# Performance work log

Hardware: AMD Instinct MI355X
Metric: run time of the kernel (lower is better)

Reference implementation:

```python
import jax, jax.numpy as jnp
import numpy as np

N, F, C1, H, C2, E = 50000, 256, 32, 8, 16, 800000
NEG_SLOPE = 0.2


def gat_layer(x, src, dst, W, a_src, a_dst, b, heads, out_c, concat):
    n = x.shape[0]
    h = (x @ W).reshape(n, heads, out_c)               # [N,H,C]
    al_src = jnp.sum(h * a_src, axis=-1)               # [N,H]
    al_dst = jnp.sum(h * a_dst, axis=-1)               # [N,H]
    e = jax.nn.leaky_relu(al_src[src] + al_dst[dst], NEG_SLOPE)  # [E,H]
    # segment softmax over incoming edges of each dst node
    m = jax.ops.segment_max(e, dst, num_segments=n)
    e = jnp.exp(e - m[dst])
    denom = jax.ops.segment_sum(e, dst, num_segments=n)
    alpha = e / (denom[dst] + 1e-16)                   # [E,H]
    msg = h[src] * alpha[..., None]                    # [E,H,C]
    out = jax.ops.segment_sum(msg, dst, num_segments=n)
    out = out.reshape(n, heads * out_c) if concat else out.mean(axis=1)
    return out + b


def conv1d(x, w, b):
    # x: [1,C,N], w: [O,I,K], 'same' padding (K=5 -> pad 2)
    pad = (w.shape[-1] - 1) // 2
    y = jax.lax.conv_general_dilated(x, w, (1,), [(pad, pad)],
                                     dimension_numbers=('NCH', 'OIH', 'NCH'))
    return y + b[None, :, None]


def setup_inputs() -> dict:
    key = jax.random.key(0)
    ks = jax.random.split(key, 20)
    s = lambda k, shp, sc: jax.random.normal(k, shp, jnp.float32) * sc
    inp = {
        'x': jax.random.normal(ks[0], (N, F), jnp.float32),
        'edge_index': jax.random.randint(ks[1], (2, E), 0, N, jnp.int32),
        'W1': s(ks[2], (F, H * C1), 0.06),
        'a_src1': s(ks[3], (H, C1), 0.1), 'a_dst1': s(ks[4], (H, C1), 0.1),
        'b1': jnp.zeros((H * C1,), jnp.float32),
        'W2': s(ks[5], (H * C1, C2), 0.06),
        'a_src2': s(ks[6], (1, C2), 0.1), 'a_dst2': s(ks[7], (1, C2), 0.1),
        'b2': jnp.zeros((C2,), jnp.float32),
        'proj_w': s(ks[8], (C2, 1), 0.2), 'proj_b': jnp.zeros((1,), jnp.float32),
        'c1_w': s(ks[9], (C2, C2, 5), 0.1), 'c1_b': jnp.zeros((C2,), jnp.float32),
        'c2_w': s(ks[10], (C2, C2, 5), 0.1), 'c2_b': jnp.zeros((C2,), jnp.float32),
        'lin_w': s(ks[11], (2 * C2, C2), 0.15), 'lin_b': jnp.zeros((C2,), jnp.float32),
    }
    return inp


def reference(x, edge_index, W1, a_src1, a_dst1, b1, W2, a_src2, a_dst2, b2,
              proj_w, proj_b, c1_w, c1_b, c2_w, c2_b, lin_w, lin_b):
    n = x.shape[0]
    loops = jnp.arange(n, dtype=edge_index.dtype)
    src = jnp.concatenate([edge_index[0], loops])  # PyG GATConv adds self-loops
    dst = jnp.concatenate([edge_index[1], loops])

    h = jax.nn.relu(gat_layer(x, src, dst, W1, a_src1, a_dst1, b1, H, C1, True))
    x1 = gat_layer(h, src, dst, W2, a_src2, a_dst2, b2, 1, C2, False)  # [N,C2]

    g = (x1 @ proj_w + proj_b)[:, 0]                  # [N]
    sort_idx = jnp.argsort(g)
    inverse_idx = jnp.argsort(sort_idx)
    sorted_x = g[sort_idx][:, None] * x1[sort_idx]    # [N,C2]
    sx = sorted_x.T[None]                             # [1,C2,N]
    sx = jax.nn.relu(conv1d(sx, c1_w, c1_b))
    sx = conv1d(sx, c2_w, c2_b)
    x2 = sx[0].T[inverse_idx]                         # [N,C2]

    out = jnp.concatenate([x1, x2], axis=1) @ lin_w + lin_b
    return jax.nn.log_softmax(out, axis=1)
```

## Files before the change

kernel.cpp:

```cpp
#include <hip/hip_runtime.h>
#include <math.h>

#define NBUCKET 65536

__device__ __forceinline__ float leakyrelu02(float v) { return v > 0.f ? v : 0.2f * v; }

__global__ __launch_bounds__(256) void k_gemm1(const float* __restrict__ A,
                                               const float* __restrict__ B,
                                               float* __restrict__ C, int M) {
  __shared__ float As[16][68];
  const int m0 = blockIdx.x * 64;
  const int n0 = blockIdx.y * 64;
  const int tid = threadIdx.x;
  const int l = tid & 63;
  const int wu = __builtin_amdgcn_readfirstlane(tid >> 6);
  const float* __restrict__ Bw = B + n0 + wu * 16;

  float acc[16];
#pragma unroll
  for (int j = 0; j < 16; ++j) acc[j] = 0.f;

  const int arow = tid & 63, akk = (tid >> 6) * 4;

  for (int k0 = 0; k0 < 256; k0 += 16) {
    float4 av = make_float4(0.f, 0.f, 0.f, 0.f);
    if (m0 + arow < M) av = *(const float4*)(A + (size_t)(m0 + arow) * 256 + k0 + akk);
    As[akk + 0][arow] = av.x;
    As[akk + 1][arow] = av.y;
    As[akk + 2][arow] = av.z;
    As[akk + 3][arow] = av.w;
    __syncthreads();
#pragma unroll
    for (int kk = 0; kk < 16; ++kk) {
      const float* bp = Bw + (size_t)(k0 + kk) * 256;
      float4 b0 = *(const float4*)(bp);
      float4 b1 = *(const float4*)(bp + 4);
      float4 b2 = *(const float4*)(bp + 8);
      float4 b3 = *(const float4*)(bp + 12);
      float a = As[kk][l];
      acc[0] += a * b0.x;  acc[1] += a * b0.y;  acc[2] += a * b0.z;  acc[3] += a * b0.w;
      acc[4] += a * b1.x;  acc[5] += a * b1.y;  acc[6] += a * b1.z;  acc[7] += a * b1.w;
      acc[8] += a * b2.x;  acc[9] += a * b2.y;  acc[10] += a * b2.z; acc[11] += a * b2.w;
      acc[12] += a * b3.x; acc[13] += a * b3.y; acc[14] += a * b3.z; acc[15] += a * b3.w;
    }
    __syncthreads();
  }
  const int m = m0 + l;
  if (m < M) {
    float* cp = C + (size_t)m * 256 + n0 + wu * 16;
    *(float4*)(cp + 0) = make_float4(acc[0], acc[1], acc[2], acc[3]);
    *(float4*)(cp + 4) = make_float4(acc[4], acc[5], acc[6], acc[7]);
    *(float4*)(cp + 8) = make_float4(acc[8], acc[9], acc[10], acc[11]);
    *(float4*)(cp + 12) = make_float4(acc[12], acc[13], acc[14], acc[15]);
  }
}

__global__ __launch_bounds__(256) void k_al1(const float* __restrict__ h_lin,
                                             const float* __restrict__ a_src,
                                             const float* __restrict__ a_dst,
                                             float* __restrict__ als,
                                             float* __restrict__ ald, int N) {
  int gid = blockIdx.x * 256 + threadIdx.x;
  int n = gid >> 6;
  int l = threadIdx.x & 63;
  if (n >= N) return;
  float4 h4 = *(const float4*)(h_lin + (size_t)n * 256 + l * 4);
  float4 vs = *(const float4*)(a_src + l * 4);
  float4 vd = *(const float4*)(a_dst + l * 4);
  float ps = h4.x * vs.x + h4.y * vs.y + h4.z * vs.z + h4.w * vs.w;
  float pd = h4.x * vd.x + h4.y * vd.y + h4.z * vd.z + h4.w * vd.w;
  ps += __shfl_xor(ps, 1); pd += __shfl_xor(pd, 1);
  ps += __shfl_xor(ps, 2); pd += __shfl_xor(pd, 2);
  ps += __shfl_xor(ps, 4); pd += __shfl_xor(pd, 4);
  if ((l & 7) == 0) {
    als[(size_t)n * 8 + (l >> 3)] = ps;
    ald[(size_t)n * 8 + (l >> 3)] = pd;
  }
}

__global__ __launch_bounds__(256) void k_hist(const int* __restrict__ ei,
                                              int* __restrict__ counts, int E, int N) {
  int e = blockIdx.x * 256 + threadIdx.x;
  if (e >= E + N) return;
  int d = (e < E) ? ei[E + e] : (e - E);
  atomicAdd(&counts[d], 1);
}

__global__ __launch_bounds__(1024) void k_scan(const int* __restrict__ counts,
                                               int* __restrict__ offsets,
                                               int* __restrict__ cursor, int chunk) {
  __shared__ int part[1024];
  const int t = threadIdx.x;
  const int base = t * chunk;
  int ssum = 0;
  for (int i = 0; i < chunk; i += 4) {
    int4 v = *(const int4*)(counts + base + i);
    ssum += v.x + v.y + v.z + v.w;
  }
  part[t] = ssum;
  __syncthreads();
  for (int d = 1; d < 1024; d <<= 1) {
    int v = (t >= d) ? part[t - d] : 0;
    __syncthreads();
    part[t] += v;
    __syncthreads();
  }
  int run = (t == 0) ? 0 : part[t - 1];
  for (int i = 0; i < chunk; i += 4) {
    int4 v = *(const int4*)(counts + base + i);
    int4 o;
    o.x = run; run += v.x;
    o.y = run; run += v.y;
    o.z = run; run += v.z;
    o.w = run; run += v.w;
    *(int4*)(offsets + base + i) = o;
    if (cursor) *(int4*)(cursor + base + i) = o;
  }
  if (t == 1023) offsets[1024 * chunk] = run;
}

__global__ __launch_bounds__(256) void k_scatter_ew(
    const int* __restrict__ ei, const float* __restrict__ als1,
    const float* __restrict__ ald1, int* __restrict__ cursor,
    int* __restrict__ csr_src, int* __restrict__ csr_dst,
    float* __restrict__ ew, int E, int N) {
  int e = blockIdx.x * 256 + threadIdx.x;
  if (e >= E + N) return;
  int d, s;
  if (e < E) { d = ei[E + e]; s = ei[e]; }
  else { d = e - E; s = d; }
  int pos = atomicAdd(&cursor[d], 1);
  csr_src[pos] = s;
  csr_dst[pos] = d;
  float4 as0 = *(const float4*)(als1 + (size_t)s * 8);
  float4 as1 = *(const float4*)(als1 + (size_t)s * 8 + 4);
  float4 ad0 = *(const float4*)(ald1 + (size_t)d * 8);
  float4 ad1 = *(const float4*)(ald1 + (size_t)d * 8 + 4);
  float4 w0, w1;
  w0.x = expf(leakyrelu02(as0.x + ad0.x));
  w0.y = expf(leakyrelu02(as0.y + ad0.y));
  w0.z = expf(leakyrelu02(as0.z + ad0.z));
  w0.w = expf(leakyrelu02(as0.w + ad0.w));
  w1.x = expf(leakyrelu02(as1.x + ad1.x));
  w1.y = expf(leakyrelu02(as1.y + ad1.y));
  w1.z = expf(leakyrelu02(as1.z + ad1.z));
  w1.w = expf(leakyrelu02(as1.w + ad1.w));
  *(float4*)(ew + (size_t)pos * 8) = w0;
  *(float4*)(ew + (size_t)pos * 8 + 4) = w1;
}

__global__ __launch_bounds__(256) void k_ew2(const int* __restrict__ csr_src,
                                             const int* __restrict__ csr_dst,
                                             const float* __restrict__ als2,
                                             const float* __restrict__ ald2,
                                             float* __restrict__ ew2, int Etot) {
  int t = blockIdx.x * 256 + threadIdx.x;
  if (t >= Etot) return;
  ew2[t] = expf(leakyrelu02(als2[csr_src[t]] + ald2[csr_dst[t]]));
}

#define RB(i) ((i) + ((i) >> 3))

__global__ __launch_bounds__(256) void k_gat1(
    const float* __restrict__ h_lin, const float* __restrict__ ew,
    const float* __restrict__ b1, const int* __restrict__ offsets,
    const int* __restrict__ csr_src, const float* __restrict__ W2,
    const float* __restrict__ a_src2, const float* __restrict__ a_dst2,
    float* __restrict__ h2, float* __restrict__ als2, float* __restrict__ ald2, int N) {
  __shared__ float rowbuf[4][292];

  const int w = threadIdx.x >> 6;
  const int l = threadIdx.x & 63;
  const int half = l >> 5;
  const int li = l & 31;
  const int h3 = li >> 2;
  const int n = blockIdx.x * 4 + w;
  if (n >= N) return;

  const int off = offsets[n];
  const int deg = offsets[n + 1] - off;
  const float* hb = h_lin + li * 8;

  float c0 = 0.f, c1 = 0.f, c2 = 0.f, c3 = 0.f, c4 = 0.f, c5 = 0.f, c6 = 0.f, c7 = 0.f;
  float sw = 0.f;
  int e = 0;
  for (; e + 8 <= deg; e += 8) {
    const int p0 = off + e + half;
    int s0 = csr_src[p0];
    int s1 = csr_src[p0 + 2];
    int s2 = csr_src[p0 + 4];
    int s3 = csr_src[p0 + 6];
    float w0 = ew[(size_t)p0 * 8 + h3];
    float w1 = ew[(size_t)(p0 + 2) * 8 + h3];
    float w2v = ew[(size_t)(p0 + 4) * 8 + h3];
    float w3 = ew[(size_t)(p0 + 6) * 8 + h3];
    const float* r0p = hb + (size_t)s0 * 256;
    const float* r1p = hb + (size_t)s1 * 256;
    const float* r2p = hb + (size_t)s2 * 256;
    const float* r3p = hb + (size_t)s3 * 256;
    float4 r0a = *(const float4*)(r0p), r0b = *(const float4*)(r0p + 4);
    float4 r1a = *(const float4*)(r1p), r1b = *(const float4*)(r1p + 4);
    float4 r2a = *(const float4*)(r2p), r2b = *(const float4*)(r2p + 4);
    float4 r3a = *(const float4*)(r3p), r3b = *(const float4*)(r3p + 4);
    sw += (w0 + w1) + (w2v + w3);
    c0 += w0 * r0a.x + w1 * r1a.x + w2v * r2a.x + w3 * r3a.x;
    c1 += w0 * r0a.y + w1 * r1a.y + w2v * r2a.y + w3 * r3a.y;
    c2 += w0 * r0a.z + w1 * r1a.z + w2v * r2a.z + w3 * r3a.z;
    c3 += w0 * r0a.w + w1 * r1a.w + w2v * r2a.w + w3 * r3a.w;
    c4 += w0 * r0b.x + w1 * r1b.x + w2v * r2b.x + w3 * r3b.x;
    c5 += w0 * r0b.y + w1 * r1b.y + w2v * r2b.y + w3 * r3b.y;
    c6 += w0 * r0b.z + w1 * r1b.z + w2v * r2b.z + w3 * r3b.z;
    c7 += w0 * r0b.w + w1 * r1b.w + w2v * r2b.w + w3 * r3b.w;
  }
  for (; e < deg; e += 2) {
    int ee = e + half;
    if (ee < deg) {
      int p = off + ee;
      int s = csr_src[p];
      float ww = ew[(size_t)p * 8 + h3];
      const float* rp = hb + (size_t)s * 256;
      float4 ra = *(const float4*)(rp), rb = *(const float4*)(rp + 4);
      sw += ww;
      c0 += ww * ra.x; c1 += ww * ra.y; c2 += ww * ra.z; c3 += ww * ra.w;
      c4 += ww * rb.x; c5 += ww * rb.y; c6 += ww * rb.z; c7 += ww * rb.w;
    }
  }
  c0 += __shfl_xor(c0, 32); c1 += __shfl_xor(c1, 32);
  c2 += __shfl_xor(c2, 32); c3 += __shfl_xor(c3, 32);
  c4 += __shfl_xor(c4, 32); c5 += __shfl_xor(c5, 32);
  c6 += __shfl_xor(c6, 32); c7 += __shfl_xor(c7, 32);
  sw += __shfl_xor(sw, 32);
  const float inv = 1.f / (sw + 1e-16f);

  if (half == 0) {
    float4 ba = *(const float4*)(b1 + li * 8);
    float4 bbv = *(const float4*)(b1 + li * 8 + 4);
    rowbuf[w][RB(li * 8 + 0)] = fmaxf(c0 * inv + ba.x, 0.f);
    rowbuf[w][RB(li * 8 + 1)] = fmaxf(c1 * inv + ba.y, 0.f);
    rowbuf[w][RB(li * 8 + 2)] = fmaxf(c2 * inv + ba.z, 0.f);
    rowbuf[w][RB(li * 8 + 3)] = fmaxf(c3 * inv + ba.w, 0.f);
    rowbuf[w][RB(li * 8 + 4)] = fmaxf(c4 * inv + bbv.x, 0.f);
    rowbuf[w][RB(li * 8 + 5)] = fmaxf(c5 * inv + bbv.y, 0.f);
    rowbuf[w][RB(li * 8 + 6)] = fmaxf(c6 * inv + bbv.z, 0.f);
    rowbuf[w][RB(li * 8 + 7)] = fmaxf(c7 * inv + bbv.w, 0.f);
  }
  asm volatile("s_waitcnt lgkmcnt(0)" ::: "memory");

  const int o = l & 15;
  const int grp = l >> 4;
  float a2 = 0.f;
#pragma unroll 8
  for (int t = 0; t < 64; ++t) {
    int cc = grp * 64 + ((t + grp * 8) & 63);
    a2 += rowbuf[w][RB(cc)] * W2[cc * 16 + o];
  }
  a2 += __shfl_xor(a2, 16);
  a2 += __shfl_xor(a2, 32);

  if (l < 16) {
    h2[(size_t)n * 16 + l] = a2;
    float ps = a2 * a_src2[l];
    float pd = a2 * a_dst2[l];
    ps += __shfl_xor(ps, 1); pd += __shfl_xor(pd, 1);
    ps += __shfl_xor(ps, 2); pd += __shfl_xor(pd, 2);
    ps += __shfl_xor(ps, 4); pd += __shfl_xor(pd, 4);
    ps += __shfl_xor(ps, 8); pd += __shfl_xor(pd, 8);
    if (l == 0) { als2[n] = ps; ald2[n] = pd; }
  }
}

__global__ __launch_bounds__(256) void k_gat2(
    const float* __restrict__ h2, const float* __restrict__ ew2,
    const float* __restrict__ b2, const float* __restrict__ proj_w,
    const float* __restrict__ proj_b, const int* __restrict__ offsets,
    const int* __restrict__ csr_src, float* __restrict__ x1,
    float* __restrict__ g, unsigned long long* __restrict__ keys,
    int* __restrict__ bhist, int N) {
  const int w = threadIdx.x >> 6;
  const int l = threadIdx.x & 63;
  const int n = blockIdx.x * 4 + w;
  if (n >= N) return;
  const int off = offsets[n];
  const int deg = offsets[n + 1] - off;
  const int slot = l >> 4;
  const int c = l & 15;

  float acc = 0.f, sw = 0.f;
  int e0 = 0;
  for (; e0 + 8 <= deg; e0 += 8) {
    int pA = off + e0 + slot;
    int pB = off + e0 + 4 + slot;
    int sA = csr_src[pA];
    int sB = csr_src[pB];
    float wA = ew2[pA];
    float wB = ew2[pB];
    float hA = h2[(size_t)sA * 16 + c];
    float hB = h2[(size_t)sB * 16 + c];
    sw += wA + wB;
    acc += wA * hA + wB * hB;
  }
  for (; e0 < deg; e0 += 4) {
    int e = e0 + slot;
    if (e < deg) {
      int p = off + e;
      int s = csr_src[p];
      float v = ew2[p];
      sw += v;
      acc += v * h2[(size_t)s * 16 + c];
    }
  }
  acc += __shfl_xor(acc, 16); sw += __shfl_xor(sw, 16);
  acc += __shfl_xor(acc, 32); sw += __shfl_xor(sw, 32);
  float x1v = acc / (sw + 1e-16f) + b2[c];

  float pg = x1v * proj_w[c];
  pg += __shfl_xor(pg, 1);
  pg += __shfl_xor(pg, 2);
  pg += __shfl_xor(pg, 4);
  pg += __shfl_xor(pg, 8);
  if (l < 16) x1[(size_t)n * 16 + l] = x1v;
  if (l == 0) {
    float gv = pg + proj_b[0];
    g[n] = gv;
    unsigned u = __float_as_uint(gv);
    u = (u & 0x80000000u) ? ~u : (u | 0x80000000u);
    keys[n] = (((unsigned long long)u) << 32) | (unsigned)n;
    atomicAdd(&bhist[u >> 16], 1);
  }
}

__global__ __launch_bounds__(256) void k_bscatter(const unsigned long long* __restrict__ keys,
                                                  int* __restrict__ cursor,
                                                  unsigned long long* __restrict__ bkeys, int N) {
  int n = blockIdx.x * 256 + threadIdx.x;
  if (n >= N) return;
  unsigned long long k = keys[n];
  int b = (int)(k >> 48);
  int pos = atomicAdd(&cursor[b], 1);
  bkeys[pos] = k;
}

__global__ __launch_bounds__(256) void k_brank(const unsigned long long* __restrict__ bkeys,
                                               const int* __restrict__ boffs,
                                               const float* __restrict__ g,
                                               const float* __restrict__ x1,
                                               int* __restrict__ rank,
                                               float* __restrict__ sortedv, int N) {
  int pos = blockIdx.x * 256 + threadIdx.x;
  if (pos >= N) return;
  unsigned long long k = bkeys[pos];
  int b = (int)(k >> 48);
  int lo = boffs[b], hi = boffs[b + 1];
  int r = lo;
  for (int j = lo; j < hi; ++j) r += (bkeys[j] < k) ? 1 : 0;
  int idx = (int)(unsigned)(k & 0xffffffffull);
  rank[idx] = r;
  float gv = g[idx];
#pragma unroll
  for (int c = 0; c < 16; c += 4) {
    float4 v = *(const float4*)(x1 + (size_t)idx * 16 + c);
    float4 o = make_float4(gv * v.x, gv * v.y, gv * v.z, gv * v.w);
    *(float4*)(sortedv + (size_t)r * 16 + c) = o;
  }
}

__global__ __launch_bounds__(256) void k_conv(const float* __restrict__ in,
                                              const float* __restrict__ wgt,
                                              const float* __restrict__ bias,
                                              float* __restrict__ out, int N, int relu) {
  __shared__ float s[260][17];
  __shared__ float ws[1280];
  __shared__ float bs[16];
  const int p0 = blockIdx.x * 256;
  for (int i = threadIdx.x; i < 1280; i += 256) ws[i] = wgt[i];
  if (threadIdx.x < 16) bs[threadIdx.x] = bias[threadIdx.x];
  for (int idx = threadIdx.x; idx < 260 * 16; idx += 256) {
    int lp = idx >> 4, c = idx & 15;
    int gp = p0 - 2 + lp;
    s[lp][c] = (gp >= 0 && gp < N) ? in[(size_t)gp * 16 + c] : 0.f;
  }
  __syncthreads();
  const int p = p0 + threadIdx.x;
  if (p >= N) return;
  float acc[16];
#pragma unroll
  for (int o = 0; o < 16; ++o) acc[o] = bs[o];
  for (int k = 0; k < 5; ++k) {
    for (int c = 0; c < 16; ++c) {
      float xv = s[threadIdx.x + k][c];
#pragma unroll
      for (int o = 0; o < 16; ++o) acc[o] += ws[(o * 16 + c) * 5 + k] * xv;
    }
  }
#pragma unroll
  for (int o = 0; o < 16; ++o) {
    float v = acc[o];
    if (relu) v = fmaxf(v, 0.f);
    out[(size_t)p * 16 + o] = v;
  }
}

__global__ __launch_bounds__(256) void k_final(
    const float* __restrict__ x1, const float* __restrict__ c2out,
    const int* __restrict__ rank, const float* __restrict__ lin_w,
    const float* __restrict__ lin_b, float* __restrict__ out, int N) {
  __shared__ float lw[512];
  __shared__ float lb[16];
  for (int i = threadIdx.x; i < 512; i += 256) lw[i] = lin_w[i];
  if (threadIdx.x < 16) lb[threadIdx.x] = lin_b[threadIdx.x];
  __syncthreads();
  const int n = blockIdx.x * 256 + threadIdx.x;
  if (n >= N) return;
  float xa[16], xb[16];
  const int r = rank[n];
#pragma unroll
  for (int c = 0; c < 16; c += 4) {
    float4 va = *(const float4*)(x1 + (size_t)n * 16 + c);
    float4 vb = *(const float4*)(c2out + (size_t)r * 16 + c);
    xa[c] = va.x; xa[c + 1] = va.y; xa[c + 2] = va.z; xa[c + 3] = va.w;
    xb[c] = vb.x; xb[c + 1] = vb.y; xb[c + 2] = vb.z; xb[c + 3] = vb.w;
  }
  float z[16];
#pragma unroll
  for (int o = 0; o < 16; ++o) z[o] = lb[o];
#pragma unroll
  for (int c = 0; c < 16; ++c) {
    float va = xa[c], vb = xb[c];
#pragma unroll
    for (int o = 0; o < 16; ++o) z[o] += va * lw[c * 16 + o] + vb * lw[(16 + c) * 16 + o];
  }
  float m = z[0];
#pragma unroll
  for (int o = 1; o < 16; ++o) m = fmaxf(m, z[o]);
  float ssum = 0.f;
#pragma unroll
  for (int o = 0; o < 16; ++o) ssum += expf(z[o] - m);
  float lse = m + logf(ssum);
#pragma unroll
  for (int o = 0; o < 16; ++o) out[(size_t)n * 16 + o] = z[o] - lse;
}

extern "C" void kernel_launch(void* const* d_in, const int* in_sizes, int n_in,
                              void* d_out, int out_size, void* d_ws, size_t ws_size,
                              hipStream_t stream) {
  const float* x = (const float*)d_in[0];
  const int* ei = (const int*)d_in[1];
  const float* W1 = (const float*)d_in[2];
  const float* a_src1 = (const float*)d_in[3];
  const float* a_dst1 = (const float*)d_in[4];
  const float* b1 = (const float*)d_in[5];
  const float* W2 = (const float*)d_in[6];
  const float* a_src2 = (const float*)d_in[7];
  const float* a_dst2 = (const float*)d_in[8];
  const float* b2 = (const float*)d_in[9];
  const float* proj_w = (const float*)d_in[10];
  const float* proj_b = (const float*)d_in[11];
  const float* c1_w = (const float*)d_in[12];
  const float* c1_b = (const float*)d_in[13];
  const float* c2_w = (const float*)d_in[14];
  const float* c2_b = (const float*)d_in[15];
  const float* lin_w = (const float*)d_in[16];
  const float* lin_b = (const float*)d_in[17];
  float* out = (float*)d_out;

  const int N = in_sizes[0] / 256;
  const int E = in_sizes[1] / 2;
  const int Etot = E + N;

  int chunk = (N + 1023) / 1024;
  chunk = (chunk + 3) & ~3;
  const int Npad = 1024 * chunk;

  char* ws = (char*)d_ws;
  size_t off = 0;
  auto alloc = [&](size_t bytes) -> void* {
    void* p = ws + off;
    off = (off + bytes + 255) & ~(size_t)255;
    return p;
  };
  float* h_lin = (float*)alloc((size_t)N * 256 * 4);
  float* als1 = (float*)alloc((size_t)N * 8 * 4);
  float* ald1 = (float*)alloc((size_t)N * 8 * 4);
  int* counts = (int*)alloc((size_t)Npad * 4);
  int* offsets = (int*)alloc((size_t)(Npad + 1) * 4);
  int* cursor = (int*)alloc((size_t)Npad * 4);
  int* csr_src = (int*)alloc((size_t)Etot * 4);
  int* csr_dst = (int*)alloc((size_t)Etot * 4);
  float* ew = (float*)alloc((size_t)Etot * 8 * 4);
  float* ew2 = (float*)alloc((size_t)Etot * 4);
  float* h2 = (float*)alloc((size_t)N * 16 * 4);
  float* als2 = (float*)alloc((size_t)N * 4);
  float* ald2 = (float*)alloc((size_t)N * 4);
  float* x1 = (float*)alloc((size_t)N * 16 * 4);
  float* gbuf = (float*)alloc((size_t)N * 4);
  unsigned long long* keys = (unsigned long long*)alloc((size_t)N * 8);
  int* bhist = (int*)alloc((size_t)NBUCKET * 4);
  int* boffs = (int*)alloc((size_t)(NBUCKET + 1) * 4);
  int* bcursor = (int*)alloc((size_t)NBUCKET * 4);
  unsigned long long* bkeys = (unsigned long long*)alloc((size_t)N * 8);
  int* rank = (int*)alloc((size_t)N * 4);
  float* sortedv = (float*)alloc((size_t)N * 16 * 4);
  float* c1out = (float*)alloc((size_t)N * 16 * 4);
  float* c2out = (float*)alloc((size_t)N * 16 * 4);
  if (off > ws_size) return;

  hipMemsetAsync(counts, 0, (size_t)Npad * 4, stream);
  hipMemsetAsync(bhist, 0, (size_t)NBUCKET * 4, stream);

  dim3 gg((N + 63) / 64, 4);
  k_gemm1<<<gg, 256, 0, stream>>>(x, W1, h_lin, N);
  k_al1<<<(N + 3) / 4, 256, 0, stream>>>(h_lin, a_src1, a_dst1, als1, ald1, N);
  k_hist<<<(Etot + 255) / 256, 256, 0, stream>>>(ei, counts, E, N);
  k_scan<<<1, 1024, 0, stream>>>(counts, offsets, cursor, chunk);
  k_scatter_ew<<<(Etot + 255) / 256, 256, 0, stream>>>(ei, als1, ald1, cursor,
                                                       csr_src, csr_dst, ew, E, N);
  k_gat1<<<(N + 3) / 4, 256, 0, stream>>>(h_lin, ew, b1, offsets, csr_src,
                                          W2, a_src2, a_dst2, h2, als2, ald2, N);
  k_ew2<<<(Etot + 255) / 256, 256, 0, stream>>>(csr_src, csr_dst, als2, ald2, ew2, Etot);
  k_gat2<<<(N + 3) / 4, 256, 0, stream>>>(h2, ew2, b2, proj_w, proj_b,
                                          offsets, csr_src, x1, gbuf, keys, bhist, N);
  k_scan<<<1, 1024, 0, stream>>>(bhist, boffs, bcursor, NBUCKET / 1024);
  k_bscatter<<<(N + 255) / 256, 256, 0, stream>>>(keys, bcursor, bkeys, N);
  k_brank<<<(N + 255) / 256, 256, 0, stream>>>(bkeys, boffs, gbuf, x1, rank, sortedv, N);
  k_conv<<<(N + 255) / 256, 256, 0, stream>>>(sortedv, c1_w, c1_b, c1out, N, 1);
  k_conv<<<(N + 255) / 256, 256, 0, stream>>>(c1out, c2_w, c2_b, c2out, N, 0);
  k_final<<<(N + 255) / 256, 256, 0, stream>>>(x1, c2out, rank, lin_w, lin_b, out, N);
}
```

Before: 539.4 us.

## Fuse attention logits into GEMM epilogue and compute layer-2 edge weights inline

The layer-1 attention dot products are now computed in the GEMM epilogue from the accumulators, with partial sums combined in shared memory, so the separate k_al1 kernel and its re-read of h_lin are gone. The k_ew2 kernel and the csr_dst array are also removed. k_gat2 now computes each edge weight on the fly from als2[src] plus the node's ald2. This saves two launches and several passes over edge-sized arrays. In exchange, k_gemm1 gains a block barrier and extra epilogue work, and k_gat2 does a gather and an exp per edge for each of its 16 channel lanes.

```diff
diff --git a/kernel.cpp b/kernel.cpp
--- a/kernel.cpp
+++ b/kernel.cpp
@@ -7,8 +7,14 @@
 
 __global__ __launch_bounds__(256) void k_gemm1(const float* __restrict__ A,
                                                const float* __restrict__ B,
-                                               float* __restrict__ C, int M) {
+                                               float* __restrict__ C,
+                                               const float* __restrict__ a_src,
+                                               const float* __restrict__ a_dst,
+                                               float* __restrict__ als,
+                                               float* __restrict__ ald, int M) {
   __shared__ float As[16][68];
+  __shared__ float pS[64][4];
+  __shared__ float pD[64][4];
   const int m0 = blockIdx.x * 64;
   const int n0 = blockIdx.y * 64;
   const int tid = threadIdx.x;
@@ -53,28 +59,25 @@
     *(float4*)(cp + 8) = make_float4(acc[8], acc[9], acc[10], acc[11]);
     *(float4*)(cp + 12) = make_float4(acc[12], acc[13], acc[14], acc[15]);
   }
-}
-
-__global__ __launch_bounds__(256) void k_al1(const float* __restrict__ h_lin,
-                                             const float* __restrict__ a_src,
-                                             const float* __restrict__ a_dst,
-                                             float* __restrict__ als,
-                                             float* __restrict__ ald, int N) {
-  int gid = blockIdx.x * 256 + threadIdx.x;
-  int n = gid >> 6;
-  int l = threadIdx.x & 63;
-  if (n >= N) return;
-  float4 h4 = *(const float4*)(h_lin + (size_t)n * 256 + l * 4);
-  float4 vs = *(const float4*)(a_src + l * 4);
-  float4 vd = *(const float4*)(a_dst + l * 4);
-  float ps = h4.x * vs.x + h4.y * vs.y + h4.z * vs.z + h4.w * vs.w;
-  float pd = h4.x * vd.x + h4.y * vd.y + h4.z * vd.z + h4.w * vd.w;
-  ps += __shfl_xor(ps, 1); pd += __shfl_xor(pd, 1);
-  ps += __shfl_xor(ps, 2); pd += __shfl_xor(pd, 2);
-  ps += __shfl_xor(ps, 4); pd += __shfl_xor(pd, 4);
-  if ((l & 7) == 0) {
-    als[(size_t)n * 8 + (l >> 3)] = ps;
-    ald[(size_t)n * 8 + (l >> 3)] = pd;
+
+  const int hseg = n0 >> 5;
+  const int aoff = (hseg + (wu >> 1)) * 32 + (wu & 1) * 16;
+  float ps = 0.f, pd = 0.f;
+#pragma unroll
+  for (int j = 0; j < 16; ++j) {
+    ps += acc[j] * a_src[aoff + j];
+    pd += acc[j] * a_dst[aoff + j];
+  }
+  pS[l][wu] = ps;
+  pD[l][wu] = pd;
+  __syncthreads();
+  if (tid < 128) {
+    int row = tid & 63, hp = tid >> 6;
+    int mm = m0 + row;
+    if (mm < M) {
+      als[(size_t)mm * 8 + hseg + hp] = pS[row][hp * 2] + pS[row][hp * 2 + 1];
+      ald[(size_t)mm * 8 + hseg + hp] = pD[row][hp * 2] + pD[row][hp * 2 + 1];
+    }
   }
 }
 
@@ -122,8 +125,7 @@
 __global__ __launch_bounds__(256) void k_scatter_ew(
     const int* __restrict__ ei, const float* __restrict__ als1,
     const float* __restrict__ ald1, int* __restrict__ cursor,
-    int* __restrict__ csr_src, int* __restrict__ csr_dst,
-    float* __restrict__ ew, int E, int N) {
+    int* __restrict__ csr_src, float* __restrict__ ew, int E, int N) {
   int e = blockIdx.x * 256 + threadIdx.x;
   if (e >= E + N) return;
   int d, s;
@@ -131,7 +133,6 @@
   else { d = e - E; s = d; }
   int pos = atomicAdd(&cursor[d], 1);
   csr_src[pos] = s;
-  csr_dst[pos] = d;
   float4 as0 = *(const float4*)(als1 + (size_t)s * 8);
   float4 as1 = *(const float4*)(als1 + (size_t)s * 8 + 4);
   float4 ad0 = *(const float4*)(ald1 + (size_t)d * 8);
@@ -147,16 +148,6 @@
   w1.w = expf(leakyrelu02(as1.w + ad1.w));
   *(float4*)(ew + (size_t)pos * 8) = w0;
   *(float4*)(ew + (size_t)pos * 8 + 4) = w1;
-}
-
-__global__ __launch_bounds__(256) void k_ew2(const int* __restrict__ csr_src,
-                                             const int* __restrict__ csr_dst,
-                                             const float* __restrict__ als2,
-                                             const float* __restrict__ ald2,
-                                             float* __restrict__ ew2, int Etot) {
-  int t = blockIdx.x * 256 + threadIdx.x;
-  if (t >= Etot) return;
-  ew2[t] = expf(leakyrelu02(als2[csr_src[t]] + ald2[csr_dst[t]]));
 }
 
 #define RB(i) ((i) + ((i) >> 3))
@@ -270,18 +261,19 @@
 }
 
 __global__ __launch_bounds__(256) void k_gat2(
-    const float* __restrict__ h2, const float* __restrict__ ew2,
-    const float* __restrict__ b2, const float* __restrict__ proj_w,
-    const float* __restrict__ proj_b, const int* __restrict__ offsets,
-    const int* __restrict__ csr_src, float* __restrict__ x1,
-    float* __restrict__ g, unsigned long long* __restrict__ keys,
-    int* __restrict__ bhist, int N) {
+    const float* __restrict__ h2, const float* __restrict__ als2,
+    const float* __restrict__ ald2, const float* __restrict__ b2,
+    const float* __restrict__ proj_w, const float* __restrict__ proj_b,
+    const int* __restrict__ offsets, const int* __restrict__ csr_src,
+    float* __restrict__ x1, float* __restrict__ g,
+    unsigned long long* __restrict__ keys, int* __restrict__ bhist, int N) {
   const int w = threadIdx.x >> 6;
   const int l = threadIdx.x & 63;
   const int n = blockIdx.x * 4 + w;
   if (n >= N) return;
   const int off = offsets[n];
   const int deg = offsets[n + 1] - off;
+  const float ad = ald2[n];
   const int slot = l >> 4;
   const int c = l & 15;
 
@@ -292,10 +284,12 @@
     int pB = off + e0 + 4 + slot;
     int sA = csr_src[pA];
     int sB = csr_src[pB];
-    float wA = ew2[pA];
-    float wB = ew2[pB];
+    float vA = als2[sA];
+    float vB = als2[sB];
     float hA = h2[(size_t)sA * 16 + c];
     float hB = h2[(size_t)sB * 16 + c];
+    float wA = expf(leakyrelu02(vA + ad));
+    float wB = expf(leakyrelu02(vB + ad));
     sw += wA + wB;
     acc += wA * hA + wB * hB;
   }
@@ -304,7 +298,7 @@
     if (e < deg) {
       int p = off + e;
       int s = csr_src[p];
-      float v = ew2[p];
+      float v = expf(leakyrelu02(als2[s] + ad));
       sw += v;
       acc += v * h2[(size_t)s * 16 + c];
     }
@@ -485,9 +479,7 @@
   int* offsets = (int*)alloc((size_t)(Npad + 1) * 4);
   int* cursor = (int*)alloc((size_t)Npad * 4);
   int* csr_src = (int*)alloc((size_t)Etot * 4);
-  int* csr_dst = (int*)alloc((size_t)Etot * 4);
   float* ew = (float*)alloc((size_t)Etot * 8 * 4);
-  float* ew2 = (float*)alloc((size_t)Etot * 4);
   float* h2 = (float*)alloc((size_t)N * 16 * 4);
   float* als2 = (float*)alloc((size_t)N * 4);
   float* ald2 = (float*)alloc((size_t)N * 4);
@@ -508,16 +500,14 @@
   hipMemsetAsync(bhist, 0, (size_t)NBUCKET * 4, stream);
 
   dim3 gg((N + 63) / 64, 4);
-  k_gemm1<<<gg, 256, 0, stream>>>(x, W1, h_lin, N);
-  k_al1<<<(N + 3) / 4, 256, 0, stream>>>(h_lin, a_src1, a_dst1, als1, ald1, N);
+  k_gemm1<<<gg, 256, 0, stream>>>(x, W1, h_lin, a_src1, a_dst1, als1, ald1, N);
   k_hist<<<(Etot + 255) / 256, 256, 0, stream>>>(ei, counts, E, N);
   k_scan<<<1, 1024, 0, stream>>>(counts, offsets, cursor, chunk);
   k_scatter_ew<<<(Etot + 255) / 256, 256, 0, stream>>>(ei, als1, ald1, cursor,
-                                                       csr_src, csr_dst, ew, E, N);
+                                                       csr_src, ew, E, N);
   k_gat1<<<(N + 3) / 4, 256, 0, stream>>>(h_lin, ew, b1, offsets, csr_src,
                                           W2, a_src2, a_dst2, h2, als2, ald2, N);
-  k_ew2<<<(Etot + 255) / 256, 256, 0, stream>>>(csr_src, csr_dst, als2, ald2, ew2, Etot);
-  k_gat2<<<(N + 3) / 4, 256, 0, stream>>>(h2, ew2, b2, proj_w, proj_b,
+  k_gat2<<<(N + 3) / 4, 256, 0, stream>>>(h2, als2, ald2, b2, proj_w, proj_b,
                                           offsets, csr_src, x1, gbuf, keys, bhist, N);
   k_scan<<<1, 1024, 0, stream>>>(bhist, boffs, bcursor, NBUCKET / 1024);
   k_bscatter<<<(N + 255) / 256, 256, 0, stream>>>(keys, bcursor, bkeys, N);
```

Result: no change. 533.9 us (median of 2 runs) (-1.0%).
